# Optimization experiments

Hardware: AMD Instinct MI355X
Metric: run time of the kernel (lower is better)

## Reference

```python
import jax, jax.numpy as jnp
import numpy as np

N_QUBITS = 4
LAYERS = 2
NUM_HEADS = 8
EMBED = 32
DK = EMBED // NUM_HEADS  # == N_QUBITS
B, S = 32, 4096


def _ry(t):
    c, s = jnp.cos(t / 2), jnp.sin(t / 2)
    m = jnp.stack([jnp.stack([c, -s], -1), jnp.stack([s, c], -1)], -2)
    return m.astype(jnp.complex64)


def _rx(t):
    c = jnp.cos(t / 2).astype(jnp.complex64)
    s = (-1j) * jnp.sin(t / 2).astype(jnp.complex64)
    return jnp.stack([jnp.stack([c, s], -1), jnp.stack([s, c], -1)], -2)


def _rz(t):
    em = jnp.exp(-0.5j * t.astype(jnp.complex64))
    ep = jnp.conj(em)
    z = jnp.zeros_like(em)
    return jnp.stack([jnp.stack([em, z], -1), jnp.stack([z, ep], -1)], -2)


def _apply_1q(state, U, w, n):
    # state: (B, 2**n); wire 0 is the most-significant bit (PennyLane convention)
    s = state.reshape(-1, 2 ** w, 2, 2 ** (n - 1 - w))
    if U.ndim == 2:  # shared gate
        s = jnp.einsum('ij,bpjq->bpiq', U, s)
    else:  # per-token gate, U: (B,2,2)
        s = jnp.einsum('bij,bpjq->bpiq', U, s)
    return s.reshape(-1, 2 ** n)


def _cnot(state, c, t, n):
    s = state.reshape((-1,) + (2,) * n)
    c_ax, t_ax = 1 + c, 1 + t
    s0 = jax.lax.slice_in_dim(s, 0, 1, axis=c_ax)
    s1 = jax.lax.slice_in_dim(s, 1, 2, axis=c_ax)
    s1 = jnp.flip(s1, axis=t_ax)  # X on target where control == 1
    s = jnp.concatenate([s0, s1], axis=c_ax)
    return s.reshape(-1, 2 ** n)


def _z_expvals(state, n):
    p = jnp.abs(state) ** 2  # (B, 2**n)
    outs = []
    for i in range(n):
        pr = p.reshape(-1, 2 ** i, 2, 2 ** (n - 1 - i))
        outs.append(pr[:, :, 0, :].sum((1, 2)) - pr[:, :, 1, :].sum((1, 2)))
    return jnp.stack(outs, -1)  # (B, n)


def _head_fwd(x_h, p_h):
    # x_h: (BT, n_qubits) angles, p_h: (layers, n_qubits, 3)
    n, L = N_QUBITS, LAYERS
    bt = x_h.shape[0]
    state = jnp.zeros((bt, 2 ** n), jnp.complex64).at[:, 0].set(1.0)
    for i in range(n):
        state = _apply_1q(state, _ry(x_h[:, i]), i, n)
    for l in range(L):
        for i in range(n):
            state = _apply_1q(state, _rx(p_h[l, i, 0]), i, n)
            state = _apply_1q(state, _ry(p_h[l, i, 1]), i, n)
            state = _apply_1q(state, _rz(p_h[l, i, 2]), i, n)
        for i in range(n - 1):
            state = _cnot(state, i, i + 1, n)
        state = _cnot(state, n - 1, 0, n)
    return _z_expvals(state, n)


def setup_inputs() -> dict:
    key = jax.random.key(0)
    k1, k2, k3, k4 = jax.random.split(key, 4)
    x = jax.random.normal(k1, (B, S, EMBED), jnp.float32)
    params = jax.random.normal(k2, (NUM_HEADS, LAYERS, N_QUBITS, 3), jnp.float32)
    fan_in = NUM_HEADS * N_QUBITS
    bound = 1.0 / np.sqrt(fan_in)
    W_out = jax.random.uniform(k3, (EMBED, fan_in), jnp.float32, -bound, bound)
    b_out = jax.random.uniform(k4, (EMBED,), jnp.float32, -bound, bound)
    return {'x': x, 'params': params, 'W_out': W_out, 'b_out': b_out}


def reference(x, params, W_out, b_out):
    b, s, e = x.shape
    xh = x.reshape(b, s, NUM_HEADS, DK)
    xh = jnp.moveaxis(xh, 2, 0).reshape(NUM_HEADS, b * s, DK)  # (H, BT, d_k)
    ang = xh[:, :, :N_QUBITS]  # angles fed into RY embedding
    ev = jax.vmap(_head_fwd)(ang, params)  # (H, BT, n_qubits)
    concat = jnp.moveaxis(ev, 0, 1).reshape(b, s, NUM_HEADS * N_QUBITS)
    return concat @ W_out.T + b_out
```

## Files before the change

### kernel.cpp

```cpp
#include <hip/hip_runtime.h>
#include <math.h>

#define NQ   4
#define NH   8
#define NL   2
#define DIM  16
#define EMB  32
#define TPB  64

#define LO_SCALE 4096.0f
#define LO_INV   (1.0f/4096.0f)

typedef _Float16 f16x8  __attribute__((ext_vector_type(8)));
typedef float    f32x16 __attribute__((ext_vector_type(16)));

__global__ void build_unitaries_kernel(const float* __restrict__ params,
                                       float* __restrict__ Uws) {
    int tid = threadIdx.x;
    int h   = tid >> 4;
    int col = tid & 15;

    float re[DIM], im[DIM];
#pragma unroll
    for (int j = 0; j < DIM; ++j) { re[j] = (j == col) ? 1.f : 0.f; im[j] = 0.f; }

#pragma unroll
    for (int l = 0; l < NL; ++l) {
#pragma unroll
        for (int q = 0; q < NQ; ++q) {
            const float* p = params + ((h * NL + l) * NQ + q) * 3;
            const int m = 1 << (3 - q);
            {
                float s, c; __sincosf(0.5f * p[0], &s, &c);
#pragma unroll
                for (int j = 0; j < DIM; ++j) {
                    if (j & m) continue;
                    const int j1 = j | m;
                    float r0 = re[j], i0 = im[j], r1 = re[j1], i1 = im[j1];
                    re[j]  = c * r0 + s * i1;
                    im[j]  = c * i0 - s * r1;
                    re[j1] = s * i0 + c * r1;
                    im[j1] = -s * r0 + c * i1;
                }
            }
            {
                float s, c; __sincosf(0.5f * p[1], &s, &c);
#pragma unroll
                for (int j = 0; j < DIM; ++j) {
                    if (j & m) continue;
                    const int j1 = j | m;
                    float r0 = re[j], i0 = im[j], r1 = re[j1], i1 = im[j1];
                    re[j]  = c * r0 - s * r1;
                    im[j]  = c * i0 - s * i1;
                    re[j1] = s * r0 + c * r1;
                    im[j1] = s * i0 + c * i1;
                }
            }
            {
                float s, c; __sincosf(0.5f * p[2], &s, &c);
#pragma unroll
                for (int j = 0; j < DIM; ++j) {
                    if (j & m) continue;
                    const int j1 = j | m;
                    float r0 = re[j], i0 = im[j], r1 = re[j1], i1 = im[j1];
                    re[j]  = c * r0 + s * i0;
                    im[j]  = c * i0 - s * r0;
                    re[j1] = c * r1 - s * i1;
                    im[j1] = c * i1 + s * r1;
                }
            }
        }
#pragma unroll
        for (int e = 0; e < NQ; ++e) {
            const int cm = 1 << (3 - e), tm = 1 << (3 - ((e + 1) & 3));
#pragma unroll
            for (int j = 0; j < DIM; ++j) {
                if ((j & cm) && !(j & tm)) {
                    const int j1 = j | tm;
                    float tr = re[j]; re[j] = re[j1]; re[j1] = tr;
                    float ti = im[j]; im[j] = im[j1]; im[j1] = ti;
                }
            }
        }
    }

    _Float16* Ah = (_Float16*)Uws;
    _Float16* Al = Ah + 4096;
    const int khigh = col >> 3, e = col & 7;
#pragma unroll
    for (int j = 0; j < DIM; ++j) {
        {
            const float v = re[j];
            const _Float16 h16 = (_Float16)v;
            const float lo = (v - (float)h16) * LO_SCALE;
            const int lane = j + 32 * khigh;
            Ah[(h * 64 + lane) * 8 + e] = h16;
            Al[(h * 64 + lane) * 8 + e] = (_Float16)lo;
        }
        {
            const float v = im[j];
            const _Float16 h16 = (_Float16)v;
            const float lo = (v - (float)h16) * LO_SCALE;
            const int lane = 16 + j + 32 * khigh;
            Ah[(h * 64 + lane) * 8 + e] = h16;
            Al[(h * 64 + lane) * 8 + e] = (_Float16)lo;
        }
    }
}

__global__ __launch_bounds__(512, 4)
void qmha_kernel(const float* __restrict__ x,
                 const float* __restrict__ Uws,
                 const float* __restrict__ W,
                 const float* __restrict__ bvec,
                 float* __restrict__ out,
                 int ntok) {
    __shared__ float evs[EMB * TPB];
    __shared__ float Wt[EMB * 36];

    const int tid  = threadIdx.x;
    const int tok0 = blockIdx.x * TPB;

    {
        const int idx = tid * 2;
        const float2 w2 = *(const float2*)(W + idx);
        const int e0 = idx >> 5, k0 = idx & 31;
        const int e1 = (idx + 1) >> 5, k1 = (idx + 1) & 31;
        Wt[k0 * 36 + e0] = w2.x;
        Wt[k1 * 36 + e1] = w2.y;
    }

    {
        const int h    = tid >> 6;
        const int lane = tid & 63;
        const int lh   = lane & 31;
        const int hi   = lane >> 5;

        const _Float16* Ah = (const _Float16*)Uws;
        const _Float16* Al = Ah + 4096;
        const f16x8 Afh = *(const f16x8*)(Ah + (h * 64 + lane) * 8);
        const f16x8 Afl = *(const f16x8*)(Al + (h * 64 + lane) * 8);

#pragma unroll
        for (int g = 0; g < 2; ++g) {
            const int t    = g * 32 + lh;
            const int tok  = tok0 + t;
            const int tokc = (tok < ntok) ? tok : (ntok - 1);

            const float4 xa = *(const float4*)(x + (size_t)tokc * EMB + h * NQ);
            float c0, s0, c1, s1, c2, s2, c3, s3;
            __sincosf(0.5f * xa.x, &s0, &c0);
            __sincosf(0.5f * xa.y, &s1, &c1);
            __sincosf(0.5f * xa.z, &s2, &c2);
            __sincosf(0.5f * xa.w, &s3, &c3);

            const float f  = hi ? s0 : c0;
            const float pA = f * c1, pB = f * s1;
            const float p23[4] = {c2 * c3, c2 * s3, s2 * c3, s2 * s3};

            f16x8 bh, bl;
#pragma unroll
            for (int e = 0; e < 8; ++e) {
                const float av = ((e >> 2) ? pB : pA) * p23[e & 3];
                const _Float16 ah16 = (_Float16)av;
                bh[e] = ah16;
                bl[e] = (_Float16)((av - (float)ah16) * LO_SCALE);
            }

            f32x16 accH, accL;
#pragma unroll
            for (int i = 0; i < 16; ++i) { accH[i] = 0.f; accL[i] = 0.f; }
            accH = __builtin_amdgcn_mfma_f32_32x32x16_f16(Afh, bh, accH, 0, 0, 0);
            accL = __builtin_amdgcn_mfma_f32_32x32x16_f16(Afl, bh, accL, 0, 0, 0);
            accL = __builtin_amdgcn_mfma_f32_32x32x16_f16(Afh, bl, accL, 0, 0, 0);

            float pj[8];
#pragma unroll
            for (int r = 0; r < 8; ++r) {
                const float ar = fmaf(accL[r],     LO_INV, accH[r]);
                const float ai = fmaf(accL[r + 8], LO_INV, accH[r + 8]);
                pj[r] = ar * ar + ai * ai;
            }
            const float s01 = pj[0] + pj[1], s23 = pj[2] + pj[3];
            const float s45 = pj[4] + pj[5], s67 = pj[6] + pj[7];
            const float sa = s01 + s23, sb = s45 + s67;
            float ev0 = sa - sb;
            const float tot = sa + sb;
            float ev1 = hi ? -tot : tot;
            float ev2 = (s01 + s45) - (s23 + s67);
            float ev3 = (pj[0] - pj[1]) + (pj[2] - pj[3]) +
                        (pj[4] - pj[5]) + (pj[6] - pj[7]);
            ev0 += __shfl_xor(ev0, 32);
            ev1 += __shfl_xor(ev1, 32);
            ev2 += __shfl_xor(ev2, 32);
            ev3 += __shfl_xor(ev3, 32);

            if (hi == 0 && tok < ntok) {
                evs[(h * 4 + 0) * TPB + t] = ev0;
                evs[(h * 4 + 1) * TPB + t] = ev1;
                evs[(h * 4 + 2) * TPB + t] = ev2;
                evs[(h * 4 + 3) * TPB + t] = ev3;
            }
        }
    }
    __syncthreads();

    {
        const int t2 = tid >> 3;
        const int eg = tid & 7;
        const int tok = tok0 + t2;
        if (tok < ntok) {
            const float4 bv = *(const float4*)(bvec + eg * 4);
            float o0 = bv.x, o1 = bv.y, o2 = bv.z, o3 = bv.w;
#pragma unroll
            for (int k = 0; k < EMB; ++k) {
                const float evk = evs[k * TPB + t2];
                const float4 wk = *(const float4*)(Wt + k * 36 + eg * 4);
                o0 = fmaf(wk.x, evk, o0);
                o1 = fmaf(wk.y, evk, o1);
                o2 = fmaf(wk.z, evk, o2);
                o3 = fmaf(wk.w, evk, o3);
            }
            float4 v; v.x = o0; v.y = o1; v.z = o2; v.w = o3;
            *(float4*)(out + (size_t)tok * EMB + eg * 4) = v;
        }
    }
}

extern "C" void kernel_launch(void* const* d_in, const int* in_sizes, int n_in,
                              void* d_out, int out_size, void* d_ws, size_t ws_size,
                              hipStream_t stream) {
    const float* x      = (const float*)d_in[0];
    const float* params = (const float*)d_in[1];
    const float* W_out  = (const float*)d_in[2];
    const float* b_out  = (const float*)d_in[3];
    float*       out    = (float*)d_out;
    float*       Uws    = (float*)d_ws;

    const int ntok = in_sizes[0] / EMB;

    hipLaunchKernelGGL(build_unitaries_kernel, dim3(1), dim3(128), 0, stream,
                       params, Uws);

    const int blocks = (ntok + TPB - 1) / TPB;
    hipLaunchKernelGGL(qmha_kernel, dim3(blocks), dim3(512), 0, stream,
                       x, Uws, W_out, b_out, out, ntok);
}
```

Baseline: 87.17 us.

## Move output projection to split-f16 MFMA and process 256 tokens per block

The output linear layer now runs on MFMA instructions using a hi/lo f16 split, replacing the per-thread scalar FMA loop. W is pre-split into f16 fragments once by the setup kernel. Tokens per block go from 64 to 256, so each wave loops over 8 token groups and the unitary fragment loads are amortized. The output stores become scalar per-lane writes instead of float4, and the larger shared buffer (32 KB) may limit occupancy.

Measured after the change: 88.09 us. No clear change (+1.1%).

```diff
diff --git a/kernel.cpp b/kernel.cpp
--- a/kernel.cpp
+++ b/kernel.cpp
@@ -6,7 +6,7 @@
 #define NL   2
 #define DIM  16
 #define EMB  32
-#define TPB  64
+#define TPB  256
 
 #define LO_SCALE 4096.0f
 #define LO_INV   (1.0f/4096.0f)
@@ -15,6 +15,7 @@
 typedef float    f32x16 __attribute__((ext_vector_type(16)));
 
 __global__ void build_unitaries_kernel(const float* __restrict__ params,
+                                       const float* __restrict__ W,
                                        float* __restrict__ Uws) {
     int tid = threadIdx.x;
     int h   = tid >> 4;
@@ -106,43 +107,52 @@
             Al[(h * 64 + lane) * 8 + e] = (_Float16)lo;
         }
     }
+
+    if (tid < 64) {
+        const int eo = tid & 31, kh = tid >> 5;
+        _Float16* Wf = ((_Float16*)Uws) + 8192 + tid * 32;
+#pragma unroll
+        for (int j = 0; j < 8; ++j) {
+            const float v0 = W[eo * EMB + kh * 8 + j];
+            const float v1 = W[eo * EMB + 16 + kh * 8 + j];
+            const _Float16 h0 = (_Float16)v0;
+            const _Float16 h1 = (_Float16)v1;
+            Wf[j]      = h0;
+            Wf[8 + j]  = h1;
+            Wf[16 + j] = (_Float16)((v0 - (float)h0) * LO_SCALE);
+            Wf[24 + j] = (_Float16)((v1 - (float)h1) * LO_SCALE);
+        }
+    }
 }
 
 __global__ __launch_bounds__(512, 4)
 void qmha_kernel(const float* __restrict__ x,
                  const float* __restrict__ Uws,
-                 const float* __restrict__ W,
                  const float* __restrict__ bvec,
                  float* __restrict__ out,
                  int ntok) {
     __shared__ float evs[EMB * TPB];
-    __shared__ float Wt[EMB * 36];
 
     const int tid  = threadIdx.x;
     const int tok0 = blockIdx.x * TPB;
+    const int lane = tid & 63;
+    const int lh   = lane & 31;
+    const int hi   = lane >> 5;
+
+    f32x16 zz;
+#pragma unroll
+    for (int i = 0; i < 16; ++i) zz[i] = 0.f;
 
     {
-        const int idx = tid * 2;
-        const float2 w2 = *(const float2*)(W + idx);
-        const int e0 = idx >> 5, k0 = idx & 31;
-        const int e1 = (idx + 1) >> 5, k1 = (idx + 1) & 31;
-        Wt[k0 * 36 + e0] = w2.x;
-        Wt[k1 * 36 + e1] = w2.y;
-    }
-
-    {
-        const int h    = tid >> 6;
-        const int lane = tid & 63;
-        const int lh   = lane & 31;
-        const int hi   = lane >> 5;
-
-        const _Float16* Ah = (const _Float16*)Uws;
-        const _Float16* Al = Ah + 4096;
-        const f16x8 Afh = *(const f16x8*)(Ah + (h * 64 + lane) * 8);
-        const f16x8 Afl = *(const f16x8*)(Al + (h * 64 + lane) * 8);
-
-#pragma unroll
-        for (int g = 0; g < 2; ++g) {
+        const int h = __builtin_amdgcn_readfirstlane(tid >> 6);
+
+        const _Float16* Ahp = (const _Float16*)Uws;
+        const _Float16* Alp = Ahp + 4096;
+        const f16x8 Afh = *(const f16x8*)(Ahp + (h * 64 + lane) * 8);
+        const f16x8 Afl = *(const f16x8*)(Alp + (h * 64 + lane) * 8);
+
+#pragma unroll 2
+        for (int g = 0; g < 8; ++g) {
             const int t    = g * 32 + lh;
             const int tok  = tok0 + t;
             const int tokc = (tok < ntok) ? tok : (ntok - 1);
@@ -167,11 +177,8 @@
                 bl[e] = (_Float16)((av - (float)ah16) * LO_SCALE);
             }
 
-            f32x16 accH, accL;
-#pragma unroll
-            for (int i = 0; i < 16; ++i) { accH[i] = 0.f; accL[i] = 0.f; }
-            accH = __builtin_amdgcn_mfma_f32_32x32x16_f16(Afh, bh, accH, 0, 0, 0);
-            accL = __builtin_amdgcn_mfma_f32_32x32x16_f16(Afl, bh, accL, 0, 0, 0);
+            f32x16 accH = __builtin_amdgcn_mfma_f32_32x32x16_f16(Afh, bh, zz, 0, 0, 0);
+            f32x16 accL = __builtin_amdgcn_mfma_f32_32x32x16_f16(Afl, bh, zz, 0, 0, 0);
             accL = __builtin_amdgcn_mfma_f32_32x32x16_f16(Afh, bl, accL, 0, 0, 0);
 
             float pj[8];
@@ -206,23 +213,44 @@
     __syncthreads();
 
     {
-        const int t2 = tid >> 3;
-        const int eg = tid & 7;
-        const int tok = tok0 + t2;
-        if (tok < ntok) {
-            const float4 bv = *(const float4*)(bvec + eg * 4);
-            float o0 = bv.x, o1 = bv.y, o2 = bv.z, o3 = bv.w;
-#pragma unroll
-            for (int k = 0; k < EMB; ++k) {
-                const float evk = evs[k * TPB + t2];
-                const float4 wk = *(const float4*)(Wt + k * 36 + eg * 4);
-                o0 = fmaf(wk.x, evk, o0);
-                o1 = fmaf(wk.y, evk, o1);
-                o2 = fmaf(wk.z, evk, o2);
-                o3 = fmaf(wk.w, evk, o3);
-            }
-            float4 v; v.x = o0; v.y = o1; v.z = o2; v.w = o3;
-            *(float4*)(out + (size_t)tok * EMB + eg * 4) = v;
+        const int w = tid >> 6;
+        const _Float16* Wf = ((const _Float16*)Uws) + 8192 + lane * 32;
+        const f16x8 Wh0 = *(const f16x8*)(Wf + 0);
+        const f16x8 Wh1 = *(const f16x8*)(Wf + 8);
+        const f16x8 Wl0 = *(const f16x8*)(Wf + 16);
+        const f16x8 Wl1 = *(const f16x8*)(Wf + 24);
+        const float bias = bvec[lh];
+
+        const float* evp = evs + w * 32 + lh;
+        f16x8 Ah0, Ah1, Al0, Al1;
+#pragma unroll
+        for (int e = 0; e < 8; ++e) {
+            const int k0 = hi * 8 + e;
+            const float v0 = evp[k0 * TPB];
+            const float v1 = evp[(16 + k0) * TPB];
+            const _Float16 a0 = (_Float16)v0;
+            const _Float16 a1 = (_Float16)v1;
+            Ah0[e] = a0;
+            Ah1[e] = a1;
+            Al0[e] = (_Float16)((v0 - (float)a0) * LO_SCALE);
+            Al1[e] = (_Float16)((v1 - (float)a1) * LO_SCALE);
+        }
+
+        f32x16 aH = __builtin_amdgcn_mfma_f32_32x32x16_f16(Ah0, Wh0, zz, 0, 0, 0);
+        aH = __builtin_amdgcn_mfma_f32_32x32x16_f16(Ah1, Wh1, aH, 0, 0, 0);
+        f32x16 aL = __builtin_amdgcn_mfma_f32_32x32x16_f16(Al0, Wh0, zz, 0, 0, 0);
+        aL = __builtin_amdgcn_mfma_f32_32x32x16_f16(Al1, Wh1, aL, 0, 0, 0);
+        aL = __builtin_amdgcn_mfma_f32_32x32x16_f16(Ah0, Wl0, aL, 0, 0, 0);
+        aL = __builtin_amdgcn_mfma_f32_32x32x16_f16(Ah1, Wl1, aL, 0, 0, 0);
+
+#pragma unroll
+        for (int r = 0; r < 16; ++r) {
+            const int trow = (r & 3) + 8 * (r >> 2) + 4 * hi;
+            const int tok  = tok0 + w * 32 + trow;
+            if (tok < ntok) {
+                out[(size_t)tok * EMB + lh] =
+                    fmaf(aL[r], LO_INV, aH[r]) + bias;
+            }
         }
     }
 }
@@ -240,9 +268,9 @@
     const int ntok = in_sizes[0] / EMB;
 
     hipLaunchKernelGGL(build_unitaries_kernel, dim3(1), dim3(128), 0, stream,
-                       params, Uws);
+                       params, W_out, Uws);
 
     const int blocks = (ntok + TPB - 1) / TPB;
     hipLaunchKernelGGL(qmha_kernel, dim3(blocks), dim3(512), 0, stream,
-                       x, Uws, W_out, b_out, out, ntok);
+                       x, Uws, b_out, out, ntok);
 }
```
